# Optimization experiments

Hardware: AMD Instinct MI355X
Metric: run time of the kernel (lower is better)

The kernel has to match this reference:

```python
import jax, jax.numpy as jnp
import numpy as np

EPS = 1e-7
MAX_NORM = 1.0 - 1e-3  # projection radius of the unit Poincare ball (c=1)
ALPHA = 0.2            # LeakyReLU negative slope
NEG_INF = -9e15


def _proj(x, max_norm=MAX_NORM):
    # Project points back inside the Poincare ball along the last dim.
    norm = jnp.clip(jnp.linalg.norm(x, axis=-1, keepdims=True), EPS)
    return jnp.where(norm > max_norm, x / norm * max_norm, x)


def _logmap0(x):
    # Log map at the origin of the Poincare ball, c = 1.
    norm = jnp.clip(jnp.linalg.norm(x, axis=-1, keepdims=True), EPS, 1.0 - EPS)
    return jnp.arctanh(norm) * x / norm


def _expmap0(v):
    # Exp map at the origin of the Poincare ball, c = 1.
    norm = jnp.clip(jnp.linalg.norm(v, axis=-1, keepdims=True), EPS)
    return jnp.tanh(norm) * v / norm


def setup_inputs() -> dict:
    key = jax.random.key(0)
    k1, k2, k3 = jax.random.split(key, 3)
    N, D = 12288, 128
    # points strictly inside the ball: ||x|| ~ 0.01*sqrt(128) ~ 0.11 < 1
    x = jax.random.normal(k1, (N, D), dtype=jnp.float32) * 0.01
    adj = jax.random.randint(k2, (N, N), 0, 2, dtype=jnp.int32)
    # attention vector a, as in init: N(0, 0.2) then proj(a, 0.9) row-wise
    a = jax.random.normal(k3, (2 * D, 1), dtype=jnp.float32) * 0.2
    a = _proj(a, 0.9)
    return {"x": x, "adj": adj, "a": a}


def reference(x, adj, a):
    D = a.shape[0] // 2
    x_tan = _logmap0(x)                       # [N, D]
    wh1 = x_tan @ a[:D]                       # [N, 1]
    wh2 = x_tan @ a[D:]                       # [N, 1]
    e = jax.nn.leaky_relu(wh1 + wh2.T, ALPHA)  # [N, N] additive scores
    scores = jnp.where(adj > 0, e, NEG_INF)
    attention = jax.nn.softmax(scores, axis=1)  # dropout omitted (eval mode)
    x_tan_prime = attention @ x_tan            # [N, D]
    return _proj(_expmap0(x_tan_prime))
```

## Files before the change

kernel.cpp:

```cpp
#include <hip/hip_runtime.h>
#include <math.h>

#define NN 12288
#define DD 128
#define EPSF 1e-7f
#define MAXNORM (1.0f - 1e-3f)

typedef __attribute__((ext_vector_type(8))) short short8_t;
typedef __attribute__((ext_vector_type(4))) short short4_t;
typedef __attribute__((ext_vector_type(4))) float float4_t;
typedef unsigned short ushort_t;

__device__ __forceinline__ unsigned short f2bf(float f) {
    unsigned int u = __builtin_bit_cast(unsigned int, f);
    unsigned int r = u + 0x7FFFu + ((u >> 16) & 1u);
    return (unsigned short)(r >> 16);
}

__global__ __launch_bounds__(128) void prep_kernel(
    const float* __restrict__ x, const float* __restrict__ a,
    ushort_t* __restrict__ xtb,
    float* __restrict__ wh1, float* __restrict__ wh2)
{
    const int r = blockIdx.x;
    const int t = threadIdx.x;
    const float xv = x[r * DD + t];
    const float a1 = a[t];
    const float a2 = a[DD + t];
    float s0 = xv * xv, s1 = xv * a1, s2 = xv * a2;
    #pragma unroll
    for (int o = 32; o > 0; o >>= 1) {
        s0 += __shfl_xor(s0, o);
        s1 += __shfl_xor(s1, o);
        s2 += __shfl_xor(s2, o);
    }
    __shared__ float red[6];
    const int w = t >> 6;
    if ((t & 63) == 0) { red[w * 3 + 0] = s0; red[w * 3 + 1] = s1; red[w * 3 + 2] = s2; }
    __syncthreads();
    const float sumsq = red[0] + red[3];
    const float d1    = red[1] + red[4];
    const float d2    = red[2] + red[5];
    const float nraw  = sqrtf(sumsq);
    const float nrm   = fminf(fmaxf(nraw, EPSF), 1.0f - EPSF);
    const float scale = atanhf(nrm) / nrm;
    xtb[(size_t)r * DD + t] = f2bf(xv * scale);
    if (t == 0) {
        wh1[r] = scale * d1;
        wh2[r] = scale * d2;
    }
}

__global__ __launch_bounds__(256) void swizzle_kernel(
    const ushort_t* __restrict__ xtb, ushort_t* __restrict__ xtB)
{
    __shared__ ushort_t raw[32 * 136];
    const int C = blockIdx.x;
    const int t = threadIdx.x;
    #pragma unroll
    for (int p = 0; p < 2; ++p) {
        const int idx = p * 256 + t;
        const int j = idx >> 4, cell = idx & 15;
        const uint4 v = *(const uint4*)(xtb + (size_t)(C * 32 + j) * DD + cell * 8);
        *(uint4*)&raw[j * 136 + cell * 8] = v;
    }
    __syncthreads();
    #pragma unroll
    for (int p = 0; p < 2; ++p) {
        const int oc = p * 256 + t;
        const int dt = oc >> 6;
        const int l6 = oc & 63;
        const int l15 = l6 & 15, q = l6 >> 4;
        short8_t v;
        #pragma unroll
        for (int e = 0; e < 8; ++e)
            v[e] = (short)raw[(q * 8 + e) * 136 + dt * 16 + l15];
        *(short8_t*)(xtB + (size_t)C * 4096 + oc * 8) = v;
    }
}

__global__ __launch_bounds__(256, 2) void attn_kernel(
    const int* __restrict__ adj,
    const ushort_t* __restrict__ xtB,
    const float* __restrict__ wh1, const float* __restrict__ wh2,
    float* __restrict__ pout, float* __restrict__ plsum, int jlen)
{
    __shared__ ushort_t p_st[4 * 4096];

    const int t = threadIdx.x;
    const int w = t >> 6, lane = t & 63;
    const int l15 = lane & 15, quad = lane >> 4;
    const int h = lane >> 5, lj = lane & 31;
    const int i0 = blockIdx.x * 128 + w * 32;
    const int s = blockIdx.y;
    const int jbase = s * jlen;
    const int wb = w * 4096;

    float wh1row[16];
    #pragma unroll
    for (int k = 0; k < 16; ++k) wh1row[k] = wh1[i0 + 2 * k + h];

    float4_t acc[2][8];
    #pragma unroll
    for (int g = 0; g < 2; ++g)
        #pragma unroll
        for (int dt = 0; dt < 8; ++dt) acc[g][dt] = (float4_t)0.0f;
    float lsr[16];
    #pragma unroll
    for (int k = 0; k < 16; ++k) lsr[k] = 0.0f;

    for (int j0 = jbase; j0 < jbase + jlen; j0 += 128) {
        int4 A[16];
        #pragma unroll
        for (int k = 0; k < 16; ++k)
            A[k] = *(const int4*)(adj + (size_t)(i0 + 2 * k + h) * NN + j0 + lj * 4);
        const float4 Wv = *(const float4*)(wh2 + j0 + lj * 4);

        #pragma unroll
        for (int k = 0; k < 16; ++k) {
            const float u0 = wh1row[k] + Wv.x;
            const float u1 = wh1row[k] + Wv.y;
            const float u2 = wh1row[k] + Wv.z;
            const float u3 = wh1row[k] + Wv.w;
            const float p0 = (A[k].x > 0) ? __expf(fmaxf(u0, 0.2f * u0)) : 0.0f;
            const float p1 = (A[k].y > 0) ? __expf(fmaxf(u1, 0.2f * u1)) : 0.0f;
            const float p2 = (A[k].z > 0) ? __expf(fmaxf(u2, 0.2f * u2)) : 0.0f;
            const float p3 = (A[k].w > 0) ? __expf(fmaxf(u3, 0.2f * u3)) : 0.0f;
            lsr[k] += (p0 + p1) + (p2 + p3);
            short4_t pk;
            pk[0] = (short)f2bf(p0); pk[1] = (short)f2bf(p1);
            pk[2] = (short)f2bf(p2); pk[3] = (short)f2bf(p3);
            const int r = 2 * k + h;
            const int idx = wb + r * 128 + (((lj >> 1) ^ (r & 15)) * 8) + (lj & 1) * 4;
            *(short4_t*)&p_st[idx] = pk;
        }

        #pragma unroll
        for (int c = 0; c < 4; ++c) {
            short8_t Bf[8];
            #pragma unroll
            for (int dt = 0; dt < 8; ++dt)
                Bf[dt] = *(const short8_t*)(
                    xtB + ((size_t)(j0 >> 5) + c) * 4096 + dt * 512 + lane * 8);
            const int cellsw = ((c * 4 + quad) ^ l15) * 8;
            const short8_t af0 = *(const short8_t*)&p_st[wb + l15 * 128 + cellsw];
            const short8_t af1 = *(const short8_t*)&p_st[wb + (16 + l15) * 128 + cellsw];
            #pragma unroll
            for (int dt = 0; dt < 8; ++dt) {
                acc[0][dt] = __builtin_amdgcn_mfma_f32_16x16x32_bf16(af0, Bf[dt], acc[0][dt], 0, 0, 0);
                acc[1][dt] = __builtin_amdgcn_mfma_f32_16x16x32_bf16(af1, Bf[dt], acc[1][dt], 0, 0, 0);
            }
        }
    }

    #pragma unroll
    for (int k = 0; k < 16; ++k) {
        float v = lsr[k];
        #pragma unroll
        for (int o = 1; o < 32; o <<= 1) v += __shfl_xor(v, o);
        if (lj == 0) plsum[(size_t)s * NN + i0 + 2 * k + h] = v;
    }

    #pragma unroll
    for (int g = 0; g < 2; ++g)
        #pragma unroll
        for (int dt = 0; dt < 8; ++dt)
            #pragma unroll
            for (int reg = 0; reg < 4; ++reg) {
                const int i = i0 + g * 16 + quad * 4 + reg;
                pout[((size_t)s * NN + i) * DD + dt * 16 + l15] = acc[g][dt][reg];
            }
}

__global__ __launch_bounds__(128) void reduce_kernel(
    const float* __restrict__ pout, const float* __restrict__ plsum,
    float* __restrict__ out, int S)
{
    const int i = blockIdx.x;
    const int t = threadIdx.x;
    float v = 0.0f;
    for (int s = 0; s < S; ++s) v += pout[((size_t)s * NN + i) * DD + t];
    float ls = 0.0f;
    for (int s = 0; s < S; ++s) ls += plsum[(size_t)s * NN + i];
    v /= ls;
    float ss = v * v;
    #pragma unroll
    for (int o = 1; o < 64; o <<= 1) ss += __shfl_xor(ss, o);
    __shared__ float r2[2];
    if ((t & 63) == 0) r2[t >> 6] = ss;
    __syncthreads();
    const float total = r2[0] + r2[1];
    const float nraw = sqrtf(total);
    const float nv   = fmaxf(nraw, EPSF);
    const float th   = tanhf(nv);
    const float ysc  = th / nv;
    const float nyr  = ysc * nraw;
    const float ny   = fmaxf(nyr, EPSF);
    const float psc  = (ny > MAXNORM) ? (MAXNORM / ny) : 1.0f;
    const float os   = ysc * psc;
    out[(size_t)i * DD + t] = v * os;
}

extern "C" void kernel_launch(void* const* d_in, const int* in_sizes, int n_in,
                              void* d_out, int out_size, void* d_ws, size_t ws_size,
                              hipStream_t stream) {
    const float* x   = (const float*)d_in[0];
    const int*   adj = (const int*)d_in[1];
    const float* a   = (const float*)d_in[2];
    float* out = (float*)d_out;

    char* ws = (char*)d_ws;
    ushort_t* xtb = (ushort_t*)ws;  ws += (size_t)NN * DD * sizeof(ushort_t);
    ushort_t* xtB = (ushort_t*)ws;  ws += (size_t)NN * DD * sizeof(ushort_t);
    float* wh1 = (float*)ws;        ws += NN * sizeof(float);
    float* wh2 = (float*)ws;        ws += NN * sizeof(float);

    const size_t fixed = (size_t)(ws - (char*)d_ws);
    const size_t perS  = (size_t)NN * DD * sizeof(float) + NN * sizeof(float);
    int S = 1;
    const int cand[5] = {8, 6, 4, 3, 2};
    for (int c = 0; c < 5; ++c) {
        if (fixed + (size_t)cand[c] * perS <= ws_size) { S = cand[c]; break; }
    }
    float* plsum = (float*)ws;      ws += (size_t)S * NN * sizeof(float);
    float* pout  = (float*)ws;

    const int jlen = NN / S;

    prep_kernel<<<NN, 128, 0, stream>>>(x, a, xtb, wh1, wh2);
    swizzle_kernel<<<NN / 32, 256, 0, stream>>>(xtb, xtB);
    attn_kernel<<<dim3(NN / 128, S), 256, 0, stream>>>(
        adj, xtB, wh1, wh2, pout, plsum, jlen);
    reduce_kernel<<<NN, 128, 0, stream>>>(pout, plsum, out, S);
}
```

Measured before the change: 977.7 us.

## Shrink attention rows per wave and double-buffer adjacency loads across column tiles

Each wave now handles 16 rows instead of 32, so a block covers 64 rows and the grid doubles. The column loop is unrolled by two and software-pipelined: the adjacency and wh2 loads for the next 128-column tile are issued before the current tile's exp/MFMA work, to hide global memory latency on the adj stream. The cost is that each xtB B-fragment is reused by half as many rows, roughly doubling B traffic from L2, and the last iteration issues a redundant wrap-around prefetch.

```diff
diff --git a/kernel.cpp b/kernel.cpp
--- a/kernel.cpp
+++ b/kernel.cpp
@@ -85,56 +85,61 @@
     const float* __restrict__ wh1, const float* __restrict__ wh2,
     float* __restrict__ pout, float* __restrict__ plsum, int jlen)
 {
-    __shared__ ushort_t p_st[4 * 4096];
+    __shared__ ushort_t p_st[4 * 2048];
 
     const int t = threadIdx.x;
     const int w = t >> 6, lane = t & 63;
     const int l15 = lane & 15, quad = lane >> 4;
     const int h = lane >> 5, lj = lane & 31;
-    const int i0 = blockIdx.x * 128 + w * 32;
+    const int i0 = blockIdx.x * 64 + w * 16;
     const int s = blockIdx.y;
     const int jbase = s * jlen;
-    const int wb = w * 4096;
-
-    float wh1row[16];
-    #pragma unroll
-    for (int k = 0; k < 16; ++k) wh1row[k] = wh1[i0 + 2 * k + h];
-
-    float4_t acc[2][8];
-    #pragma unroll
-    for (int g = 0; g < 2; ++g)
-        #pragma unroll
-        for (int dt = 0; dt < 8; ++dt) acc[g][dt] = (float4_t)0.0f;
-    float lsr[16];
-    #pragma unroll
-    for (int k = 0; k < 16; ++k) lsr[k] = 0.0f;
-
-    for (int j0 = jbase; j0 < jbase + jlen; j0 += 128) {
-        int4 A[16];
-        #pragma unroll
-        for (int k = 0; k < 16; ++k)
-            A[k] = *(const int4*)(adj + (size_t)(i0 + 2 * k + h) * NN + j0 + lj * 4);
-        const float4 Wv = *(const float4*)(wh2 + j0 + lj * 4);
-
-        #pragma unroll
-        for (int k = 0; k < 16; ++k) {
-            const float u0 = wh1row[k] + Wv.x;
-            const float u1 = wh1row[k] + Wv.y;
-            const float u2 = wh1row[k] + Wv.z;
-            const float u3 = wh1row[k] + Wv.w;
-            const float p0 = (A[k].x > 0) ? __expf(fmaxf(u0, 0.2f * u0)) : 0.0f;
-            const float p1 = (A[k].y > 0) ? __expf(fmaxf(u1, 0.2f * u1)) : 0.0f;
-            const float p2 = (A[k].z > 0) ? __expf(fmaxf(u2, 0.2f * u2)) : 0.0f;
-            const float p3 = (A[k].w > 0) ? __expf(fmaxf(u3, 0.2f * u3)) : 0.0f;
+    const int jend  = jbase + jlen;
+    const int wb = w * 2048;
+
+    float wh1row[8];
+    #pragma unroll
+    for (int k = 0; k < 8; ++k) wh1row[k] = wh1[i0 + 2 * k + h];
+
+    float4_t acc[8];
+    #pragma unroll
+    for (int dt = 0; dt < 8; ++dt) acc[dt] = (float4_t)0.0f;
+    float lsr[8];
+    #pragma unroll
+    for (int k = 0; k < 8; ++k) lsr[k] = 0.0f;
+
+    int4 A0[8], A1[8];
+    float4 W0, W1;
+
+    #pragma unroll
+    for (int k = 0; k < 8; ++k)
+        A0[k] = *(const int4*)(adj + (size_t)(i0 + 2 * k + h) * NN + jbase + lj * 4);
+    W0 = *(const float4*)(wh2 + jbase + lj * 4);
+
+    for (int j0 = jbase; j0 < jend; j0 += 256) {
+        #pragma unroll
+        for (int k = 0; k < 8; ++k)
+            A1[k] = *(const int4*)(adj + (size_t)(i0 + 2 * k + h) * NN + (j0 + 128) + lj * 4);
+        W1 = *(const float4*)(wh2 + (j0 + 128) + lj * 4);
+
+        #pragma unroll
+        for (int k = 0; k < 8; ++k) {
+            const float u0 = wh1row[k] + W0.x;
+            const float u1 = wh1row[k] + W0.y;
+            const float u2 = wh1row[k] + W0.z;
+            const float u3 = wh1row[k] + W0.w;
+            const float p0 = (A0[k].x > 0) ? __expf(fmaxf(u0, 0.2f * u0)) : 0.0f;
+            const float p1 = (A0[k].y > 0) ? __expf(fmaxf(u1, 0.2f * u1)) : 0.0f;
+            const float p2 = (A0[k].z > 0) ? __expf(fmaxf(u2, 0.2f * u2)) : 0.0f;
+            const float p3 = (A0[k].w > 0) ? __expf(fmaxf(u3, 0.2f * u3)) : 0.0f;
             lsr[k] += (p0 + p1) + (p2 + p3);
             short4_t pk;
             pk[0] = (short)f2bf(p0); pk[1] = (short)f2bf(p1);
             pk[2] = (short)f2bf(p2); pk[3] = (short)f2bf(p3);
             const int r = 2 * k + h;
-            const int idx = wb + r * 128 + (((lj >> 1) ^ (r & 15)) * 8) + (lj & 1) * 4;
+            const int idx = wb + r * 128 + (((lj >> 1) ^ r) * 8) + (lj & 1) * 4;
             *(short4_t*)&p_st[idx] = pk;
         }
-
         #pragma unroll
         for (int c = 0; c < 4; ++c) {
             short8_t Bf[8];
@@ -142,19 +147,53 @@
             for (int dt = 0; dt < 8; ++dt)
                 Bf[dt] = *(const short8_t*)(
                     xtB + ((size_t)(j0 >> 5) + c) * 4096 + dt * 512 + lane * 8);
-            const int cellsw = ((c * 4 + quad) ^ l15) * 8;
-            const short8_t af0 = *(const short8_t*)&p_st[wb + l15 * 128 + cellsw];
-            const short8_t af1 = *(const short8_t*)&p_st[wb + (16 + l15) * 128 + cellsw];
-            #pragma unroll
-            for (int dt = 0; dt < 8; ++dt) {
-                acc[0][dt] = __builtin_amdgcn_mfma_f32_16x16x32_bf16(af0, Bf[dt], acc[0][dt], 0, 0, 0);
-                acc[1][dt] = __builtin_amdgcn_mfma_f32_16x16x32_bf16(af1, Bf[dt], acc[1][dt], 0, 0, 0);
-            }
-        }
-    }
-
-    #pragma unroll
-    for (int k = 0; k < 16; ++k) {
+            const short8_t af = *(const short8_t*)&p_st[wb + l15 * 128 + (((c * 4 + quad) ^ l15) * 8)];
+            #pragma unroll
+            for (int dt = 0; dt < 8; ++dt)
+                acc[dt] = __builtin_amdgcn_mfma_f32_16x16x32_bf16(af, Bf[dt], acc[dt], 0, 0, 0);
+        }
+
+        int jn = j0 + 256; if (jn >= jend) jn = jbase;
+        #pragma unroll
+        for (int k = 0; k < 8; ++k)
+            A0[k] = *(const int4*)(adj + (size_t)(i0 + 2 * k + h) * NN + jn + lj * 4);
+        W0 = *(const float4*)(wh2 + jn + lj * 4);
+
+        const int j1 = j0 + 128;
+        #pragma unroll
+        for (int k = 0; k < 8; ++k) {
+            const float u0 = wh1row[k] + W1.x;
+            const float u1 = wh1row[k] + W1.y;
+            const float u2 = wh1row[k] + W1.z;
+            const float u3 = wh1row[k] + W1.w;
+            const float p0 = (A1[k].x > 0) ? __expf(fmaxf(u0, 0.2f * u0)) : 0.0f;
+            const float p1 = (A1[k].y > 0) ? __expf(fmaxf(u1, 0.2f * u1)) : 0.0f;
+            const float p2 = (A1[k].z > 0) ? __expf(fmaxf(u2, 0.2f * u2)) : 0.0f;
+            const float p3 = (A1[k].w > 0) ? __expf(fmaxf(u3, 0.2f * u3)) : 0.0f;
+            lsr[k] += (p0 + p1) + (p2 + p3);
+            short4_t pk;
+            pk[0] = (short)f2bf(p0); pk[1] = (short)f2bf(p1);
+            pk[2] = (short)f2bf(p2); pk[3] = (short)f2bf(p3);
+            const int r = 2 * k + h;
+            const int idx = wb + r * 128 + (((lj >> 1) ^ r) * 8) + (lj & 1) * 4;
+            *(short4_t*)&p_st[idx] = pk;
+        }
+        #pragma unroll
+        for (int c = 0; c < 4; ++c) {
+            short8_t Bf[8];
+            #pragma unroll
+            for (int dt = 0; dt < 8; ++dt)
+                Bf[dt] = *(const short8_t*)(
+                    xtB + ((size_t)(j1 >> 5) + c) * 4096 + dt * 512 + lane * 8);
+            const short8_t af = *(const short8_t*)&p_st[wb + l15 * 128 + (((c * 4 + quad) ^ l15) * 8)];
+            #pragma unroll
+            for (int dt = 0; dt < 8; ++dt)
+                acc[dt] = __builtin_amdgcn_mfma_f32_16x16x32_bf16(af, Bf[dt], acc[dt], 0, 0, 0);
+        }
+    }
+
+    #pragma unroll
+    for (int k = 0; k < 8; ++k) {
         float v = lsr[k];
         #pragma unroll
         for (int o = 1; o < 32; o <<= 1) v += __shfl_xor(v, o);
@@ -162,14 +201,12 @@
     }
 
     #pragma unroll
-    for (int g = 0; g < 2; ++g)
-        #pragma unroll
-        for (int dt = 0; dt < 8; ++dt)
-            #pragma unroll
-            for (int reg = 0; reg < 4; ++reg) {
-                const int i = i0 + g * 16 + quad * 4 + reg;
-                pout[((size_t)s * NN + i) * DD + dt * 16 + l15] = acc[g][dt][reg];
-            }
+    for (int dt = 0; dt < 8; ++dt)
+        #pragma unroll
+        for (int reg = 0; reg < 4; ++reg) {
+            const int i = i0 + quad * 4 + reg;
+            pout[((size_t)s * NN + i) * DD + dt * 16 + l15] = acc[dt][reg];
+        }
 }
 
 __global__ __launch_bounds__(128) void reduce_kernel(
@@ -229,7 +266,7 @@
 
     prep_kernel<<<NN, 128, 0, stream>>>(x, a, xtb, wh1, wh2);
     swizzle_kernel<<<NN / 32, 256, 0, stream>>>(xtb, xtB);
-    attn_kernel<<<dim3(NN / 128, S), 256, 0, stream>>>(
+    attn_kernel<<<dim3(NN / 64, S), 256, 0, stream>>>(
         adj, xtB, wh1, wh2, pout, plsum, jlen);
     reduce_kernel<<<NN, 128, 0, stream>>>(pout, plsum, out, S);
 }
```

After: 1.089 ms. 11.4% more time.

## Stage 512-column value tiles in LDS and compute P directly in MFMA registers

Applied to the files above, without the earlier changes.

The attention kernel is restructured so each block loads a 512-column window of the swizzled bf16 values into 128 KB of LDS once, then reuses it across 384 rows split into 16-row tiles per wave. Probabilities are computed straight into MFMA A-fragment registers instead of going through a shared P staging buffer. Adjacency and wh2 loads are double-buffered in registers across steps. The split count is raised (up to 24) and the grid reshaped. The trade-off is lower occupancy from the large LDS footprint, plus read-modify-write of partial outputs in global memory across sub-windows.

```diff
diff --git a/kernel.cpp b/kernel.cpp
--- a/kernel.cpp
+++ b/kernel.cpp
@@ -7,7 +7,6 @@
 #define MAXNORM (1.0f - 1e-3f)
 
 typedef __attribute__((ext_vector_type(8))) short short8_t;
-typedef __attribute__((ext_vector_type(4))) short short4_t;
 typedef __attribute__((ext_vector_type(4))) float float4_t;
 typedef unsigned short ushort_t;
 
@@ -79,97 +78,127 @@
     }
 }
 
-__global__ __launch_bounds__(256, 2) void attn_kernel(
+__global__ __launch_bounds__(256) void attn_kernel(
     const int* __restrict__ adj,
     const ushort_t* __restrict__ xtB,
     const float* __restrict__ wh1, const float* __restrict__ wh2,
-    float* __restrict__ pout, float* __restrict__ plsum, int jlen)
-{
-    __shared__ ushort_t p_st[4 * 4096];
+    float* __restrict__ pout, float* __restrict__ plsum, int S)
+{
+    __shared__ __align__(16) ushort_t B_lds[512 * 128];
 
     const int t = threadIdx.x;
     const int w = t >> 6, lane = t & 63;
     const int l15 = lane & 15, quad = lane >> 4;
-    const int h = lane >> 5, lj = lane & 31;
-    const int i0 = blockIdx.x * 128 + w * 32;
     const int s = blockIdx.y;
-    const int jbase = s * jlen;
-    const int wb = w * 4096;
-
-    float wh1row[16];
-    #pragma unroll
-    for (int k = 0; k < 16; ++k) wh1row[k] = wh1[i0 + 2 * k + h];
-
-    float4_t acc[2][8];
-    #pragma unroll
-    for (int g = 0; g < 2; ++g)
-        #pragma unroll
-        for (int dt = 0; dt < 8; ++dt) acc[g][dt] = (float4_t)0.0f;
-    float lsr[16];
-    #pragma unroll
-    for (int k = 0; k < 16; ++k) lsr[k] = 0.0f;
-
-    for (int j0 = jbase; j0 < jbase + jlen; j0 += 128) {
-        int4 A[16];
-        #pragma unroll
-        for (int k = 0; k < 16; ++k)
-            A[k] = *(const int4*)(adj + (size_t)(i0 + 2 * k + h) * NN + j0 + lj * 4);
-        const float4 Wv = *(const float4*)(wh2 + j0 + lj * 4);
-
-        #pragma unroll
-        for (int k = 0; k < 16; ++k) {
-            const float u0 = wh1row[k] + Wv.x;
-            const float u1 = wh1row[k] + Wv.y;
-            const float u2 = wh1row[k] + Wv.z;
-            const float u3 = wh1row[k] + Wv.w;
-            const float p0 = (A[k].x > 0) ? __expf(fmaxf(u0, 0.2f * u0)) : 0.0f;
-            const float p1 = (A[k].y > 0) ? __expf(fmaxf(u1, 0.2f * u1)) : 0.0f;
-            const float p2 = (A[k].z > 0) ? __expf(fmaxf(u2, 0.2f * u2)) : 0.0f;
-            const float p3 = (A[k].w > 0) ? __expf(fmaxf(u3, 0.2f * u3)) : 0.0f;
-            lsr[k] += (p0 + p1) + (p2 + p3);
-            short4_t pk;
-            pk[0] = (short)f2bf(p0); pk[1] = (short)f2bf(p1);
-            pk[2] = (short)f2bf(p2); pk[3] = (short)f2bf(p3);
-            const int r = 2 * k + h;
-            const int idx = wb + r * 128 + (((lj >> 1) ^ (r & 15)) * 8) + (lj & 1) * 4;
-            *(short4_t*)&p_st[idx] = pk;
+    const int jwin = NN / S;
+    const int nsub = jwin >> 9;
+    const int i_chunk = blockIdx.x * 384;
+
+    for (int sub = 0; sub < nsub; ++sub) {
+        const int jw = s * jwin + (sub << 9);
+        if (sub) __syncthreads();
+        {
+            const uint4* src = (const uint4*)(xtB + (size_t)(jw >> 5) * 4096);
+            uint4* dst = (uint4*)B_lds;
+            #pragma unroll
+            for (int m = 0; m < 32; ++m) dst[m * 256 + t] = src[m * 256 + t];
         }
-
-        #pragma unroll
-        for (int c = 0; c < 4; ++c) {
-            short8_t Bf[8];
+        __syncthreads();
+
+        int4   Ab[2][4][2];
+        float4 Wb[2][4][2];
+
+        {
+            const int i0 = i_chunk + w * 16;
+            const size_t rb = (size_t)(i0 + l15) * NN + jw + quad * 8;
+            const int wb2 = jw + quad * 8;
             #pragma unroll
-            for (int dt = 0; dt < 8; ++dt)
-                Bf[dt] = *(const short8_t*)(
-                    xtB + ((size_t)(j0 >> 5) + c) * 4096 + dt * 512 + lane * 8);
-            const int cellsw = ((c * 4 + quad) ^ l15) * 8;
-            const short8_t af0 = *(const short8_t*)&p_st[wb + l15 * 128 + cellsw];
-            const short8_t af1 = *(const short8_t*)&p_st[wb + (16 + l15) * 128 + cellsw];
+            for (int kc = 0; kc < 4; ++kc)
+                #pragma unroll
+                for (int e = 0; e < 2; ++e) {
+                    Ab[0][kc][e] = *(const int4*)(adj + rb + kc * 32 + e * 4);
+                    Wb[0][kc][e] = *(const float4*)(wh2 + wb2 + kc * 32 + e * 4);
+                }
+        }
+
+        float4_t acc[8];
+        float lsum = 0.0f;
+        float wh1i = 0.0f;
+
+        for (int step = 0; step < 24; ++step) {
+            const int it = step >> 2, q = step & 3;
+            const int cur = step & 1, nxt = cur ^ 1;
+
+            {
+                const int ns = (step < 23) ? step + 1 : step;
+                const int nit = ns >> 2, nq = ns & 3;
+                const int i0n = i_chunk + (w + 4 * nit) * 16;
+                const size_t rb = (size_t)(i0n + l15) * NN + jw + nq * 128 + quad * 8;
+                const int wb2 = jw + nq * 128 + quad * 8;
+                #pragma unroll
+                for (int kc = 0; kc < 4; ++kc)
+                    #pragma unroll
+                    for (int e = 0; e < 2; ++e) {
+                        Ab[nxt][kc][e] = *(const int4*)(adj + rb + kc * 32 + e * 4);
+                        Wb[nxt][kc][e] = *(const float4*)(wh2 + wb2 + kc * 32 + e * 4);
+                    }
+            }
+
+            const int i0 = i_chunk + (w + 4 * it) * 16;
+            if (q == 0) {
+                #pragma unroll
+                for (int dt = 0; dt < 8; ++dt) acc[dt] = (float4_t)0.0f;
+                lsum = 0.0f;
+                wh1i = wh1[i0 + l15];
+            }
+
             #pragma unroll
-            for (int dt = 0; dt < 8; ++dt) {
-                acc[0][dt] = __builtin_amdgcn_mfma_f32_16x16x32_bf16(af0, Bf[dt], acc[0][dt], 0, 0, 0);
-                acc[1][dt] = __builtin_amdgcn_mfma_f32_16x16x32_bf16(af1, Bf[dt], acc[1][dt], 0, 0, 0);
+            for (int kc = 0; kc < 4; ++kc) {
+                short8_t af;
+                #pragma unroll
+                for (int e = 0; e < 2; ++e) {
+                    const int4   A = Ab[cur][kc][e];
+                    const float4 W = Wb[cur][kc][e];
+                    const float u0 = wh1i + W.x, u1 = wh1i + W.y;
+                    const float u2 = wh1i + W.z, u3 = wh1i + W.w;
+                    const float p0 = (A.x > 0) ? __expf(fmaxf(u0, 0.2f * u0)) : 0.0f;
+                    const float p1 = (A.y > 0) ? __expf(fmaxf(u1, 0.2f * u1)) : 0.0f;
+                    const float p2 = (A.z > 0) ? __expf(fmaxf(u2, 0.2f * u2)) : 0.0f;
+                    const float p3 = (A.w > 0) ? __expf(fmaxf(u3, 0.2f * u3)) : 0.0f;
+                    lsum += (p0 + p1) + (p2 + p3);
+                    af[e * 4 + 0] = (short)f2bf(p0);
+                    af[e * 4 + 1] = (short)f2bf(p1);
+                    af[e * 4 + 2] = (short)f2bf(p2);
+                    af[e * 4 + 3] = (short)f2bf(p3);
+                }
+                const int cb = (q * 4 + kc) * 4096;
+                #pragma unroll
+                for (int dt = 0; dt < 8; ++dt) {
+                    const short8_t Bf = *(const short8_t*)&B_lds[cb + dt * 512 + lane * 8];
+                    acc[dt] = __builtin_amdgcn_mfma_f32_16x16x32_bf16(af, Bf, acc[dt], 0, 0, 0);
+                }
+            }
+
+            if (q == 3) {
+                float v = lsum;
+                v += __shfl_xor(v, 16);
+                v += __shfl_xor(v, 32);
+                if (quad == 0) {
+                    float* lp = plsum + (size_t)s * NN + i0 + l15;
+                    if (sub == 0) *lp = v; else *lp += v;
+                }
+                #pragma unroll
+                for (int dt = 0; dt < 8; ++dt)
+                    #pragma unroll
+                    for (int reg = 0; reg < 4; ++reg) {
+                        float* op = pout + ((size_t)s * NN + i0 + quad * 4 + reg) * DD
+                                    + dt * 16 + l15;
+                        if (sub == 0) *op = acc[dt][reg];
+                        else         *op += acc[dt][reg];
+                    }
             }
         }
     }
-
-    #pragma unroll
-    for (int k = 0; k < 16; ++k) {
-        float v = lsr[k];
-        #pragma unroll
-        for (int o = 1; o < 32; o <<= 1) v += __shfl_xor(v, o);
-        if (lj == 0) plsum[(size_t)s * NN + i0 + 2 * k + h] = v;
-    }
-
-    #pragma unroll
-    for (int g = 0; g < 2; ++g)
-        #pragma unroll
-        for (int dt = 0; dt < 8; ++dt)
-            #pragma unroll
-            for (int reg = 0; reg < 4; ++reg) {
-                const int i = i0 + g * 16 + quad * 4 + reg;
-                pout[((size_t)s * NN + i) * DD + dt * 16 + l15] = acc[g][dt][reg];
-            }
 }
 
 __global__ __launch_bounds__(128) void reduce_kernel(
@@ -218,18 +247,16 @@
     const size_t fixed = (size_t)(ws - (char*)d_ws);
     const size_t perS  = (size_t)NN * DD * sizeof(float) + NN * sizeof(float);
     int S = 1;
-    const int cand[5] = {8, 6, 4, 3, 2};
-    for (int c = 0; c < 5; ++c) {
+    const int cand[7] = {24, 12, 8, 6, 4, 3, 2};
+    for (int c = 0; c < 7; ++c) {
         if (fixed + (size_t)cand[c] * perS <= ws_size) { S = cand[c]; break; }
     }
     float* plsum = (float*)ws;      ws += (size_t)S * NN * sizeof(float);
     float* pout  = (float*)ws;
 
-    const int jlen = NN / S;
-
     prep_kernel<<<NN, 128, 0, stream>>>(x, a, xtb, wh1, wh2);
     swizzle_kernel<<<NN / 32, 256, 0, stream>>>(xtb, xtB);
-    attn_kernel<<<dim3(NN / 128, S), 256, 0, stream>>>(
-        adj, xtB, wh1, wh2, pout, plsum, jlen);
+    attn_kernel<<<dim3(NN / 384, S), 256, 0, stream>>>(
+        adj, xtB, wh1, wh2, pout, plsum, S);
     reduce_kernel<<<NN, 128, 0, stream>>>(pout, plsum, out, S);
 }
```

After: 1.437 ms. +47.0%, slower.
